# Optimization experiments

Measured on AMD Instinct MI355X. Metric: run time of the kernel, lower is better.

The kernel has to match this reference:

```python
import jax, jax.numpy as jnp
import numpy as np

NUM_MOLECULES = 262144
NUM_ATOMS = 8388608
MAX_ATOMIC_NUMBER = 100

SELF_ENERGIES = [(1, -0.6), (6, -38.1), (7, -54.7), (8, -75.2), (9, -99.8),
                 (16, -398.1), (17, -460.1), (35, -2573.8), (53, -297.8), (99, -1000.0)]


def setup_inputs() -> dict:
    key = jax.random.key(0)
    k1, k2, k3 = jax.random.split(key, 3)
    energy_readout = jax.random.normal(k1, (NUM_MOLECULES,), dtype=jnp.float32)
    atomic_numbers = jax.random.randint(k2, (NUM_ATOMS,), 0, MAX_ATOMIC_NUMBER, dtype=jnp.int64 if jax.config.jax_enable_x64 else jnp.int32).astype(jnp.int32)
    atomic_subsystem_indices = jnp.sort(jax.random.randint(k3, (NUM_ATOMS,), 0, NUM_MOLECULES).astype(jnp.int32))
    # learned/constant parameter: self-energy lookup table, sized max_atomic_number+1-ish (here 100)
    se = np.zeros((MAX_ATOMIC_NUMBER,), dtype=np.float32)
    for z, ase in SELF_ENERGIES:
        se[z] = ase
    self_energies_tensor = jnp.asarray(se)
    return {
        "energy_readout": energy_readout,
        "atomic_numbers": atomic_numbers,
        "atomic_subsystem_indices": atomic_subsystem_indices,
        "self_energies_tensor": self_energies_tensor,
    }


def reference(energy_readout, atomic_numbers, atomic_subsystem_indices, self_energies_tensor):
    # gather per-atom self energies, then segment-sum into per-molecule totals
    atom_self_energies = self_energies_tensor[atomic_numbers]  # [num_atoms]
    molecule_self_energies = jax.ops.segment_sum(
        atom_self_energies, atomic_subsystem_indices,
        num_segments=energy_readout.shape[0], indices_are_sorted=True)
    return energy_readout + molecule_self_energies
```

## Files before the change

kernel.cpp:

```cpp
#include <hip/hip_runtime.h>
#include <hip/hip_bf16.h>

#define NUM_MOLECULES 262144
#define NUM_ATOMS     8388608
#define TABLE_SIZE    100
#define BLOCK         256
#define CPT           8

__global__ void init_out_kernel(const float* __restrict__ energy,
                                float* __restrict__ out, int n4) {
    int i = blockIdx.x * blockDim.x + threadIdx.x;
    if (i < n4) {
        reinterpret_cast<float4*>(out)[i] =
            reinterpret_cast<const float4*>(energy)[i];
    }
}

__global__ void __launch_bounds__(BLOCK)
accum_kernel(const int* __restrict__ atomic_numbers,
             const int* __restrict__ mol_idx,
             const float* __restrict__ table,
             float* __restrict__ out) {
    __shared__ float tab[TABLE_SIZE];
    if (threadIdx.x < TABLE_SIZE) tab[threadIdx.x] = table[threadIdx.x];
    __syncthreads();

    const int tid = blockIdx.x * blockDim.x + threadIdx.x;
    const int4* zp = reinterpret_cast<const int4*>(atomic_numbers);
    const int4* mp = reinterpret_cast<const int4*>(mol_idx);
    const int4 zzA = zp[2 * tid], zzB = zp[2 * tid + 1];
    const int4 mmA = mp[2 * tid], mmB = mp[2 * tid + 1];

    const int m_all[8] = {mmA.x, mmA.y, mmA.z, mmA.w, mmB.x, mmB.y, mmB.z, mmB.w};
    const float v_all[8] = {tab[zzA.x], tab[zzA.y], tab[zzA.z], tab[zzA.w],
                            tab[zzB.x], tab[zzB.y], tab[zzB.z], tab[zzB.w]};

    int   curm = m_all[0];
    float run  = v_all[0];
    float head_sum = 0.0f;
    int   nbound = 0;
#pragma unroll
    for (int j = 1; j < CPT; ++j) {
        if (m_all[j] == curm) {
            run += v_all[j];
        } else {
            if (nbound == 0) head_sum = run;
            else atomicAdd(out + curm, run);
            ++nbound;
            curm = m_all[j];
            run  = v_all[j];
        }
    }
    const int   head_mol = m_all[0];
    const int   tail_mol = curm;
    const float tail_sum = run;

    const int lane = threadIdx.x & 63;

    const int prev_tail = __shfl_up(tail_mol, 1);
    const bool connect = (lane > 0) && (head_mol == prev_tail);
    const bool open = (nbound == 0) && connect;

    float c = tail_sum;
    int   f = open ? 0 : 1;
#pragma unroll
    for (int d = 1; d < 64; d <<= 1) {
        float cp = __shfl_up(c, d);
        int   fp = __shfl_up(f, d);
        if (lane >= d && !f) {
            c += cp;
            f |= fp;
        }
    }

    const float cin = __shfl_up(c, 1);
    if (nbound > 0) {
        atomicAdd(out + head_mol, head_sum + (connect ? cin : 0.0f));
    }

    const int next_connect = __shfl_down((int)connect, 1);
    const bool chain_end = (lane == 63) || !next_connect;
    if (chain_end) {
        atomicAdd(out + tail_mol, c);
    }
}

extern "C" void kernel_launch(void* const* d_in, const int* in_sizes, int n_in,
                              void* d_out, int out_size, void* d_ws, size_t ws_size,
                              hipStream_t stream) {
    const float* energy_readout = (const float*)d_in[0];
    const int*   atomic_numbers = (const int*)d_in[1];
    const int*   mol_idx        = (const int*)d_in[2];
    const float* table          = (const float*)d_in[3];
    float* out = (float*)d_out;

    int n4 = NUM_MOLECULES / 4;
    int b1 = 256;
    int g1 = (n4 + b1 - 1) / b1;
    init_out_kernel<<<g1, b1, 0, stream>>>(energy_readout, out, n4);

    int g2 = NUM_ATOMS / (BLOCK * CPT);
    accum_kernel<<<g2, BLOCK, 0, stream>>>(atomic_numbers, mol_idx, table, out);
}
```

Before: 99.48 us.

## Accumulate per-block molecule sums in shared memory instead of wave scans

Replaces the wave-level segmented shuffle scan and its per-chain global atomics with block-wide accumulation into a shared-memory slot array indexed by molecule offset. Molecules lying strictly inside a block's tile are written directly as energy plus sum, and only the two boundary molecules use global atomics. The aim is to cut global atomic traffic and scan overhead. In exchange it adds shared-memory atomics, an extra barrier, 8 KB of LDS per block, and a global-atomic fallback path when a block spans too many molecules. The init kernel is kept.

```diff
diff --git a/kernel.cpp b/kernel.cpp
--- a/kernel.cpp
+++ b/kernel.cpp
@@ -6,6 +6,8 @@
 #define TABLE_SIZE    100
 #define BLOCK         256
 #define CPT           8
+#define TILE          (BLOCK * CPT)
+#define SLOTS         TILE
 
 __global__ void init_out_kernel(const float* __restrict__ energy,
                                 float* __restrict__ out, int n4) {
@@ -20,68 +22,69 @@
 accum_kernel(const int* __restrict__ atomic_numbers,
              const int* __restrict__ mol_idx,
              const float* __restrict__ table,
+             const float* __restrict__ energy,
              float* __restrict__ out) {
     __shared__ float tab[TABLE_SIZE];
-    if (threadIdx.x < TABLE_SIZE) tab[threadIdx.x] = table[threadIdx.x];
-    __syncthreads();
+    __shared__ float sums[SLOTS];
+    __shared__ int s_first, s_last;
 
-    const int tid = blockIdx.x * blockDim.x + threadIdx.x;
+    const int tidx = threadIdx.x;
+    if (tidx < TABLE_SIZE) tab[tidx] = table[tidx];
+#pragma unroll
+    for (int k = 0; k < SLOTS / BLOCK; ++k)
+        sums[k * BLOCK + tidx] = 0.0f;
+
+    const int gtid = blockIdx.x * BLOCK + tidx;
     const int4* zp = reinterpret_cast<const int4*>(atomic_numbers);
     const int4* mp = reinterpret_cast<const int4*>(mol_idx);
-    const int4 zzA = zp[2 * tid], zzB = zp[2 * tid + 1];
-    const int4 mmA = mp[2 * tid], mmB = mp[2 * tid + 1];
+    const int4 zzA = zp[2 * gtid], zzB = zp[2 * gtid + 1];
+    const int4 mmA = mp[2 * gtid], mmB = mp[2 * gtid + 1];
 
-    const int m_all[8] = {mmA.x, mmA.y, mmA.z, mmA.w, mmB.x, mmB.y, mmB.z, mmB.w};
+    if (tidx == 0)         s_first = mmA.x;
+    if (tidx == BLOCK - 1) s_last  = mmB.w;
+    __syncthreads();
+    const int first = s_first;
+    const int last  = s_last;
+    const int span1 = last - first + 1;
+
+    const int   m_all[8] = {mmA.x, mmA.y, mmA.z, mmA.w, mmB.x, mmB.y, mmB.z, mmB.w};
     const float v_all[8] = {tab[zzA.x], tab[zzA.y], tab[zzA.z], tab[zzA.w],
                             tab[zzB.x], tab[zzB.y], tab[zzB.z], tab[zzB.w]};
 
-    int   curm = m_all[0];
-    float run  = v_all[0];
-    float head_sum = 0.0f;
-    int   nbound = 0;
+    if (span1 <= SLOTS) {
+        int   curm = m_all[0];
+        float run  = v_all[0];
 #pragma unroll
-    for (int j = 1; j < CPT; ++j) {
-        if (m_all[j] == curm) {
-            run += v_all[j];
-        } else {
-            if (nbound == 0) head_sum = run;
-            else atomicAdd(out + curm, run);
-            ++nbound;
-            curm = m_all[j];
-            run  = v_all[j];
+        for (int j = 1; j < CPT; ++j) {
+            if (m_all[j] == curm) {
+                run += v_all[j];
+            } else {
+                atomicAdd(&sums[curm - first], run);
+                curm = m_all[j];
+                run  = v_all[j];
+            }
         }
-    }
-    const int   head_mol = m_all[0];
-    const int   tail_mol = curm;
-    const float tail_sum = run;
+        atomicAdd(&sums[curm - first], run);
+        __syncthreads();
 
-    const int lane = threadIdx.x & 63;
-
-    const int prev_tail = __shfl_up(tail_mol, 1);
-    const bool connect = (lane > 0) && (head_mol == prev_tail);
-    const bool open = (nbound == 0) && connect;
-
-    float c = tail_sum;
-    int   f = open ? 0 : 1;
+        for (int i = tidx + 1; i < span1 - 1; i += BLOCK)
+            out[first + i] = energy[first + i] + sums[i];
+        if (tidx == 0) atomicAdd(out + first, sums[0]);
+        if (tidx == 1 && last > first) atomicAdd(out + last, sums[span1 - 1]);
+    } else {
+        int   curm = m_all[0];
+        float run  = v_all[0];
 #pragma unroll
-    for (int d = 1; d < 64; d <<= 1) {
-        float cp = __shfl_up(c, d);
-        int   fp = __shfl_up(f, d);
-        if (lane >= d && !f) {
-            c += cp;
-            f |= fp;
+        for (int j = 1; j < CPT; ++j) {
+            if (m_all[j] == curm) {
+                run += v_all[j];
+            } else {
+                atomicAdd(out + curm, run);
+                curm = m_all[j];
+                run  = v_all[j];
+            }
         }
-    }
-
-    const float cin = __shfl_up(c, 1);
-    if (nbound > 0) {
-        atomicAdd(out + head_mol, head_sum + (connect ? cin : 0.0f));
-    }
-
-    const int next_connect = __shfl_down((int)connect, 1);
-    const bool chain_end = (lane == 63) || !next_connect;
-    if (chain_end) {
-        atomicAdd(out + tail_mol, c);
+        atomicAdd(out + curm, run);
     }
 }
 
@@ -99,6 +102,7 @@
     int g1 = (n4 + b1 - 1) / b1;
     init_out_kernel<<<g1, b1, 0, stream>>>(energy_readout, out, n4);
 
-    int g2 = NUM_ATOMS / (BLOCK * CPT);
-    accum_kernel<<<g2, BLOCK, 0, stream>>>(atomic_numbers, mol_idx, table, out);
+    int g2 = NUM_ATOMS / TILE;
+    accum_kernel<<<g2, BLOCK, 0, stream>>>(atomic_numbers, mol_idx, table,
+                                           energy_readout, out);
 }
```

After: 102.7 us. 3.3% more time.
